# Kernel optimization log

Hardware: AMD Instinct MI355X
Metric: run time of the kernel (lower is better)

## Reference

```python
import jax, jax.numpy as jnp
import numpy as np
from jax import lax

IMG_SIZE = 1024.0  # nominal image dimension for generating plausible coords
IOU_THRESHOLD = 0.5


def box_iou(a, b):
    # a: (N,4), b: (M,4) in (x1,y1,x2,y2); returns (N,M) IoU
    area_a = (a[:, 2] - a[:, 0]) * (a[:, 3] - a[:, 1])
    area_b = (b[:, 2] - b[:, 0]) * (b[:, 3] - b[:, 1])
    lt = jnp.maximum(a[:, None, :2], b[None, :, :2])
    rb = jnp.minimum(a[:, None, 2:], b[None, :, 2:])
    wh = jnp.clip(rb - lt, 0.0)
    inter = wh[..., 0] * wh[..., 1]
    return inter / (area_a[:, None] + area_b[None, :] - inter)


def apply_deltas_to_locations(deltas, locations, stride):
    # Faithful to fcos_apply_deltas_to_locations: clip deltas at 0,
    # un-normalize by stride, subtract/add around the center location.
    d = jnp.clip(deltas, 0.0)  # (N,4) = (l, t, r, b)
    xc, yc = locations[:, 0], locations[:, 1]
    x1 = xc - stride * d[:, 0]
    y1 = yc - stride * d[:, 1]
    x2 = xc + stride * d[:, 2]
    y2 = yc + stride * d[:, 3]
    return jnp.stack([x1, y1, x2, y2], axis=1)


def nms_keep(boxes, scores, iou_threshold):
    # Greedy NMS, equivalent to the sequential reference loop:
    # process boxes in decreasing score order; a box survives if it is not
    # suppressed (IoU > thr) by any earlier surviving box.
    n = boxes.shape[0]
    order = jnp.argsort(-scores)  # descending score order
    b = boxes[order]
    iou = box_iou(b, b)  # (N,N), memory-bound pairwise compare
    idx = jnp.arange(n)

    def body(i, keep):
        suppress = (iou[i] > iou_threshold) & (idx > i) & keep[i]
        return keep & ~suppress

    keep_sorted = lax.fori_loop(0, n, body, jnp.ones((n,), dtype=bool))
    # scatter keep mask back to original ordering
    keep_orig = jnp.zeros((n,), dtype=bool).at[order].set(keep_sorted)
    return keep_orig, order, keep_sorted


def setup_inputs() -> dict:
    key = jax.random.key(0)
    k1, k2, k3, k4 = jax.random.split(key, 4)
    N = 8192
    deltas = jax.random.uniform(k1, (N, 4), dtype=jnp.float32) * 8.0  # stride-normalized LTRB
    locations = jax.random.uniform(k2, (N, 2), dtype=jnp.float32) * IMG_SIZE
    scores = jax.random.uniform(k3, (N,), dtype=jnp.float32)
    class_ids = jax.random.randint(k4, (N,), 0, 80, dtype=jnp.int32)
    return {"deltas": deltas, "locations": locations, "scores": scores,
            "class_ids": class_ids, "stride": 8}


def reference(deltas, locations, scores, class_ids, stride):
    # 1) LTRB delta decode (fcos_apply_deltas_to_locations)
    boxes = apply_deltas_to_locations(deltas, locations, stride)
    # 2) class-specific NMS (class_spec_nms): offset boxes per class so that
    #    boxes of different classes never overlap, then run plain NMS.
    max_coordinate = boxes.max()
    offsets = class_ids.astype(boxes.dtype) * (max_coordinate + 1.0)
    boxes_for_nms = boxes + offsets[:, None]
    keep_orig, order, keep_sorted = nms_keep(boxes_for_nms, scores, IOU_THRESHOLD)
    # boxes: decoded boxes; keep_orig: NMS survival mask (original order);
    # order: score-descending permutation (kept indices = order[keep_sorted])
    return boxes, keep_orig, order
```

## Files before the change

### kernel.cpp

```cpp
#include <hip/hip_runtime.h>

typedef unsigned long long u64;
typedef unsigned int u32;

#define NBOX 8192
#define NW64 128
#define NCLASS 80
#define NCMAX 256
#define CHKCAP 256
#define NS 32
#define SLICE 256
#define NBLK 32
#define K1GRID (NS * NBLK + 1)
#define K2GRID (NBLK + NCLASS)

__device__ __forceinline__ u32 f32_mono(float f) {
  u32 u = __float_as_uint(f);
  return (u & 0x80000000u) ? ~u : (u | 0x80000000u);
}
__device__ __forceinline__ float mono_f32(u32 u) {
  u32 b = (u & 0x80000000u) ? (u ^ 0x80000000u) : ~u;
  return __uint_as_float(b);
}
__device__ __forceinline__ u64 readlane64(u64 v, int l) {
  u32 lo = __builtin_amdgcn_readlane((u32)v, l);
  u32 hi = __builtin_amdgcn_readlane((u32)(v >> 32), l);
  return ((u64)hi << 32) | (u64)lo;
}
__device__ __forceinline__ u32 reduce_bmax(const u32* __restrict__ bmax, int t) {
  u32 bm = bmax[t & 31];
#pragma unroll
  for (int off = 16; off > 0; off >>= 1) {
    u32 o = __shfl_xor(bm, off);
    bm = (bm > o) ? bm : o;
  }
  return bm;
}


__global__ __launch_bounds__(256) void rank_decode_kernel(
    const float* __restrict__ scores, const int* __restrict__ class_ids,
    const float4* __restrict__ deltas, const float2* __restrict__ locs,
    const int* __restrict__ stride_p, float4* __restrict__ boxes_out,
    u32* __restrict__ bmax, int* __restrict__ flag, int* __restrict__ rankp) {
  const int t = threadIdx.x;
  const int b = blockIdx.x;

  if (b == NS * NBLK) {
    __shared__ float4 bxA[CHKCAP], bxB[CHKCAP];
    __shared__ int clsA[CHKCAP], clsB[CHKCAP];
    __shared__ int na, nb, hitf;
    __shared__ u32 mred[4];
    if (t == 0) { na = 0; nb = 0; hitf = 0; }
    float s = (float)(*stride_p);
    u32 mymax = 0;
    for (int base = 0; base < NBOX; base += 256) {
      int i = base + t;
      float4 d = deltas[i];
      d.x = fmaxf(d.x, 0.f); d.y = fmaxf(d.y, 0.f);
      d.z = fmaxf(d.z, 0.f); d.w = fmaxf(d.w, 0.f);
      float2 c = locs[i];
      float x1 = c.x - s * d.x, y1 = c.y - s * d.y;
      float x2 = c.x + s * d.z, y2 = c.y + s * d.w;
      float m = fmaxf(fmaxf(x1, y1), fmaxf(x2, y2));
      u32 u = f32_mono(m);
      mymax = mymax > u ? mymax : u;
    }
#pragma unroll
    for (int off = 32; off > 0; off >>= 1) {
      u32 o = __shfl_xor(mymax, off);
      mymax = mymax > o ? mymax : o;
    }
    if ((t & 63) == 0) mred[t >> 6] = mymax;
    __syncthreads();
    u32 g0 = mred[0] > mred[1] ? mred[0] : mred[1];
    u32 g1 = mred[2] > mred[3] ? mred[2] : mred[3];
    float M = mono_f32(g0 > g1 ? g0 : g1);
    float thrA = M - 65.0f;
    for (int base = 0; base < NBOX; base += 256) {
      int i = base + t;
      float4 d = deltas[i];
      d.x = fmaxf(d.x, 0.f); d.y = fmaxf(d.y, 0.f);
      d.z = fmaxf(d.z, 0.f); d.w = fmaxf(d.w, 0.f);
      float2 c = locs[i];
      float4 bb;
      bb.x = c.x - s * d.x; bb.y = c.y - s * d.y;
      bb.z = c.x + s * d.z; bb.w = c.y + s * d.w;
      int cls = class_ids[i];
      if (bb.z > thrA && bb.w > thrA) {
        int p = atomicAdd(&na, 1);
        if (p < CHKCAP) { bxA[p] = bb; clsA[p] = cls; }
      }
      if (bb.x < 1.0f && bb.y < 1.0f) {
        int p = atomicAdd(&nb, 1);
        if (p < CHKCAP) { bxB[p] = bb; clsB[p] = cls; }
      }
    }
    __syncthreads();
    int NA = na < CHKCAP ? na : CHKCAP;
    int NB = nb < CHKCAP ? nb : CHKCAP;
    bool hit = (t == 0) && (na > CHKCAP || nb > CHKCAP);
    for (int pr = t; pr < NA * NB; pr += 256) {
      int a = pr / NB, b2 = pr % NB;
      if (clsB[b2] != clsA[a] + 1) continue;
      float offa = (float)clsA[a] * (M + 1.0f);
      float offb = (float)clsB[b2] * (M + 1.0f);
      float4 A = bxA[a], Bb = bxB[b2];
      A.x += offa; A.y += offa; A.z += offa; A.w += offa;
      Bb.x += offb; Bb.y += offb; Bb.z += offb; Bb.w += offb;
      float ltx = fmaxf(A.x, Bb.x), lty = fmaxf(A.y, Bb.y);
      float rbx = fminf(A.z, Bb.z), rby = fminf(A.w, Bb.w);
      float ww = fmaxf(rbx - ltx, 0.f), hh = fmaxf(rby - lty, 0.f);
      float inter = ww * hh;
      float aa = (A.z - A.x) * (A.w - A.y);
      float ab = (Bb.z - Bb.x) * (Bb.w - Bb.y);
      float iou = inter / (aa + ab - inter);
      if (iou > 0.4f) hit = true;
    }
    if (hit) atomicOr(&hitf, 1);
    __syncthreads();
    if (t == 0) *flag = hitf;
    return;
  }

  const int bi = b & 31;
  const int slice = b >> 5;
  const int i = bi * 256 + t;

  __shared__ u32 st[SLICE];
  __shared__ u32 wmax[4];

  if (slice == 0) {
    float s = (float)(*stride_p);
    float4 d = deltas[i];
    d.x = fmaxf(d.x, 0.f); d.y = fmaxf(d.y, 0.f);
    d.z = fmaxf(d.z, 0.f); d.w = fmaxf(d.w, 0.f);
    float2 c = locs[i];
    float4 bb;
    bb.x = c.x - s * d.x;
    bb.y = c.y - s * d.y;
    bb.z = c.x + s * d.z;
    bb.w = c.y + s * d.w;
    boxes_out[i] = bb;
    float m = fmaxf(fmaxf(bb.x, bb.y), fmaxf(bb.z, bb.w));
    u32 u = f32_mono(m);
#pragma unroll
    for (int off = 32; off > 0; off >>= 1) {
      u32 o = __shfl_xor(u, off);
      u = (u > o) ? u : o;
    }
    if ((t & 63) == 0) wmax[t >> 6] = u;
  }

  st[t] = f32_mono(scores[slice * 256 + t]);
  __syncthreads();
  if (slice == 0 && t == 0) {
    u32 m0 = wmax[0] > wmax[1] ? wmax[0] : wmax[1];
    u32 m1 = wmax[2] > wmax[3] ? wmax[2] : wmax[3];
    bmax[bi] = m0 > m1 ? m0 : m1;
  }

  u32 mi = f32_mono(scores[i]);
  int tp = i - slice * 256;
  int cnt = 0;
#pragma unroll 8
  for (int p = 0; p < SLICE; ++p) {
    u32 mj = st[p];
    bool less = (mj > mi) || (mj == mi && p < tp);
    cnt += less ? 1 : 0;
  }
  rankp[slice * NBOX + i] = cnt;
}

__global__ __launch_bounds__(256) void scatter_nms_kernel(
    const float* __restrict__ scores, const int* __restrict__ class_ids,
    const float4* __restrict__ boxes, const u32* __restrict__ bmax,
    const int* __restrict__ rankp, u64* __restrict__ keys,
    float4* __restrict__ bnms, float* __restrict__ order_out,
    float* __restrict__ keep_out, int* flag) {
  const int t = threadIdx.x;
  const int bid = blockIdx.x;

  if (bid < NBLK) {
    int i = bid * 256 + t;
    int r = 0;
#pragma unroll
    for (int s2 = 0; s2 < NS; ++s2) r += rankp[s2 * NBOX + i];
    float maxc = mono_f32(reduce_bmax(bmax, t));
    u32 mi = f32_mono(scores[i]);
    keys[r] = ((u64)(~mi) << 32) | (u32)i;
    int cls = class_ids[i];
    float off = (float)cls * (maxc + 1.0f);
    float4 bb = boxes[i];
    bb.x += off; bb.y += off; bb.z += off; bb.w += off;
    bnms[r] = bb;
    order_out[r] = (float)i;
    return;
  }

  const int c = bid - NBLK;
  if (*flag != 0) return;
  __shared__ u64 ck[NCMAX];
  __shared__ u32 slist[NCMAX];
  __shared__ float4 bx[NCMAX];
  __shared__ u64 smask[NCMAX][4];
  __shared__ int cnt_s;
  if (t == 0) cnt_s = 0;
  __syncthreads();

  {
    int nxtc = class_ids[t];
    float nxts = scores[t];
    for (int base = 0; base < NBOX; base += 256) {
      int cur = nxtc;
      float cs = nxts;
      if (base + 256 < NBOX) {
        nxtc = class_ids[base + 256 + t];
        nxts = scores[base + 256 + t];
      }
      if (cur == c) {
        int p = atomicAdd(&cnt_s, 1);
        if (p < NCMAX) ck[p] = ((u64)(~f32_mono(cs)) << 32) | (u32)(base + t);
      }
    }
  }
  __syncthreads();
  int nc = cnt_s;
  if (nc > NCMAX) {
    if (t == 0) atomicOr(flag, 1);
    return;
  }
  if (t < nc) {
    u64 kme = ck[t];
    int r2 = 0;
    for (int p = 0; p < nc; ++p) r2 += (ck[p] < kme) ? 1 : 0;
    slist[r2] = (u32)kme;
  }
  __syncthreads();

  float maxc = mono_f32(reduce_bmax(bmax, t));
  float off = (float)c * (maxc + 1.0f);
  for (int k = t; k < nc; k += 256) {
    float4 bb = boxes[slist[k]];
    bb.x += off; bb.y += off; bb.z += off; bb.w += off;
    bx[k] = bb;
  }
  __syncthreads();

  {
    const int wv = t >> 6;
    const int lane = t & 63;
    const int nw = (nc + 63) >> 6;
    for (int i = wv; i < nc; i += 4) {
      float4 bi = bx[i];
      float area_i = (bi.z - bi.x) * (bi.w - bi.y);
      for (int w = 0; w < nw; ++w) {
        int j2 = w * 64 + lane;
        float4 bj = bx[j2 < NCMAX ? j2 : 0];
        float ltx = fmaxf(bi.x, bj.x), lty = fmaxf(bi.y, bj.y);
        float rbx = fminf(bi.z, bj.z), rby = fminf(bi.w, bj.w);
        float ww = fmaxf(rbx - ltx, 0.f), hh = fmaxf(rby - lty, 0.f);
        float inter = ww * hh;
        float area_j = (bj.z - bj.x) * (bj.w - bj.y);
        float iou = inter / (area_i + area_j - inter);
        bool p = (iou > 0.5f) && (j2 > i) && (j2 < nc);
        u64 mm = __ballot(p);
        if (lane == 0) smask[i][w] = mm;
      }
    }
  }
  __syncthreads();
  if (t >= 64) return;

  u64 ma[4], mb[4], mc[4], md[4];
#pragma unroll
  for (int w = 0; w < 4; ++w) {
    ma[w] = smask[t][w];
    mb[w] = smask[64 + t][w];
    mc[w] = smask[128 + t][w];
    md[w] = smask[192 + t][w];
  }
  u64 R0 = 0, R1 = 0, R2 = 0, R3 = 0;
  u64 K0 = 0, K1 = 0, K2 = 0, K3 = 0;

#define SCAND(D, MD, RD, KD)                                                   \
  {                                                                            \
    int lim = nc - (D) * 64;                                                   \
    if (lim > 0) {                                                             \
      if (lim > 64) lim = 64;                                                  \
      for (int ii = 0; ii < lim; ++ii) {                                       \
        u64 kb = ((RD >> ii) & 1ull) ^ 1ull;                                   \
        KD |= kb << ii;                                                        \
        u64 sm2 = 0ull - kb;                                                   \
        R0 |= readlane64(MD[0], ii) & sm2;                                     \
        R1 |= readlane64(MD[1], ii) & sm2;                                     \
        R2 |= readlane64(MD[2], ii) & sm2;                                     \
        R3 |= readlane64(MD[3], ii) & sm2;                                     \
      }                                                                        \
    }                                                                          \
  }
  SCAND(0, ma, R0, K0)
  SCAND(1, mb, R1, K1)
  SCAND(2, mc, R2, K2)
  SCAND(3, md, R3, K3)
#undef SCAND

  u64 kk[4] = {K0, K1, K2, K3};
#pragma unroll
  for (int d = 0; d < 4; ++d) {
    int j = d * 64 + t;
    if (j < nc) keep_out[slist[j]] = ((kk[d] >> t) & 1ull) ? 1.0f : 0.0f;
  }
}

__global__ __launch_bounds__(256) void fallback_kernel(
    const float4* __restrict__ bnms, const u64* __restrict__ keys,
    float* __restrict__ keep_out, const int* __restrict__ flag) {
  if (*flag == 0) return;
  __shared__ u64 remv[NW64];
  int t = threadIdx.x;
  for (int k = t; k < NW64; k += 256) remv[k] = 0;
  __syncthreads();
  if (t < 64) {
    int lane = t;
    for (int ii = 0; ii < NBOX; ++ii) {
      if ((remv[ii >> 6] >> (ii & 63)) & 1ull) continue;
      float4 bi = bnms[ii];
      float area_i = (bi.z - bi.x) * (bi.w - bi.y);
      for (int jb = ii + 1; jb < NBOX; jb += 64) {
        int j = jb + lane;
        bool p = false;
        if (j < NBOX) {
          float4 bj = bnms[j];
          float ltx = fmaxf(bi.x, bj.x), lty = fmaxf(bi.y, bj.y);
          float rbx = fminf(bi.z, bj.z), rby = fminf(bi.w, bj.w);
          float ww = fmaxf(rbx - ltx, 0.f), hh = fmaxf(rby - lty, 0.f);
          float inter = ww * hh;
          float area_j = (bj.z - bj.x) * (bj.w - bj.y);
          float iou = inter / (area_i + area_j - inter);
          p = iou > 0.5f;
        }
        u64 m = __ballot(p);
        if (lane == 0 && m) {
          int w0 = jb >> 6, sh = jb & 63;
          remv[w0] |= (m << sh);
          if (sh && (w0 + 1) < NW64) remv[w0 + 1] |= (m >> (64 - sh));
        }
      }
    }
  }
  __syncthreads();
  for (int k = t; k < NBOX; k += 256)
    keep_out[(u32)keys[k]] = ((remv[k >> 6] >> (k & 63)) & 1ull) ? 0.0f : 1.0f;
}

extern "C" void kernel_launch(void* const* d_in, const int* in_sizes, int n_in,
                              void* d_out, int out_size, void* d_ws, size_t ws_size,
                              hipStream_t stream) {
  const float* deltas = (const float*)d_in[0];
  const float* locs = (const float*)d_in[1];
  const float* scores = (const float*)d_in[2];
  const int* class_ids = (const int*)d_in[3];
  const int* stride_p = (const int*)d_in[4];

  float* boxes_out = (float*)d_out;
  float* keep_out = (float*)d_out + (size_t)NBOX * 4;
  float* order_out = (float*)d_out + (size_t)NBOX * 5;

  u32* bmax = (u32*)((char*)d_ws + 64);
  int* flag = (int*)((char*)d_ws + 256);
  u64* keys = (u64*)((char*)d_ws + 4096);
  float4* bnms = (float4*)((char*)d_ws + 4096 + 65536);
  int* rankp = (int*)((char*)d_ws + 4096 + 65536 + 131072);

  rank_decode_kernel<<<K1GRID, 256, 0, stream>>>(
      scores, class_ids, (const float4*)deltas, (const float2*)locs, stride_p,
      (float4*)boxes_out, bmax, flag, rankp);

  scatter_nms_kernel<<<K2GRID, 256, 0, stream>>>(
      scores, class_ids, (const float4*)boxes_out, bmax, rankp, keys, bnms,
      order_out, keep_out, flag);

  fallback_kernel<<<1, 256, 0, stream>>>(bnms, keys, keep_out, flag);
}
```

Measured before the change: 52.74 us.

## Build per-class sorted lists during ranking instead of rescanning all boxes per class

The ranking pass now also counts, for each box, how many same-class boxes outrank it, and a histogram pass records per-class counts. The scatter kernel uses these to write each box into a per-class list already in score order. The per-class NMS blocks then read their list directly instead of scanning all 8192 class ids and doing an in-block rank sort. The price is extra compare work and extra rank-partial traffic in the rank kernel, plus splitting scatter and NMS into separate launches.

```diff
diff --git a/kernel.cpp b/kernel.cpp
--- a/kernel.cpp
+++ b/kernel.cpp
@@ -6,13 +6,14 @@
 #define NBOX 8192
 #define NW64 128
 #define NCLASS 80
+#define MAXC 512
 #define NCMAX 256
 #define CHKCAP 256
 #define NS 32
 #define SLICE 256
 #define NBLK 32
 #define K1GRID (NS * NBLK + 1)
-#define K2GRID (NBLK + NCLASS)
+#define K3GRID (NCLASS + 1)
 
 __device__ __forceinline__ u32 f32_mono(float f) {
   u32 u = __float_as_uint(f);
@@ -42,16 +43,19 @@
     const float* __restrict__ scores, const int* __restrict__ class_ids,
     const float4* __restrict__ deltas, const float2* __restrict__ locs,
     const int* __restrict__ stride_p, float4* __restrict__ boxes_out,
-    u32* __restrict__ bmax, int* __restrict__ flag, int* __restrict__ rankp) {
+    u32* __restrict__ bmax, int* __restrict__ flag, int* __restrict__ ccount,
+    int* __restrict__ rankp, int* __restrict__ rcp) {
   const int t = threadIdx.x;
   const int b = blockIdx.x;
 
   if (b == NS * NBLK) {
     __shared__ float4 bxA[CHKCAP], bxB[CHKCAP];
     __shared__ int clsA[CHKCAP], clsB[CHKCAP];
+    __shared__ int hist[NCLASS];
     __shared__ int na, nb, hitf;
     __shared__ u32 mred[4];
     if (t == 0) { na = 0; nb = 0; hitf = 0; }
+    if (t < NCLASS) hist[t] = 0;
     float s = (float)(*stride_p);
     u32 mymax = 0;
     for (int base = 0; base < NBOX; base += 256) {
@@ -87,6 +91,7 @@
       bb.x = c.x - s * d.x; bb.y = c.y - s * d.y;
       bb.z = c.x + s * d.z; bb.w = c.y + s * d.w;
       int cls = class_ids[i];
+      atomicAdd(&hist[cls], 1);
       if (bb.z > thrA && bb.w > thrA) {
         int p = atomicAdd(&na, 1);
         if (p < CHKCAP) { bxA[p] = bb; clsA[p] = cls; }
@@ -97,6 +102,10 @@
       }
     }
     __syncthreads();
+    if (t < NCLASS) {
+      ccount[t] = hist[t];
+      if (hist[t] > NCMAX) atomicOr(&hitf, 1);
+    }
     int NA = na < CHKCAP ? na : CHKCAP;
     int NB = nb < CHKCAP ? nb : CHKCAP;
     bool hit = (t == 0) && (na > CHKCAP || nb > CHKCAP);
@@ -127,7 +136,7 @@
   const int slice = b >> 5;
   const int i = bi * 256 + t;
 
-  __shared__ u32 st[SLICE];
+  __shared__ u64 kt[SLICE];
   __shared__ u32 wmax[4];
 
   if (slice == 0) {
@@ -152,7 +161,10 @@
     if ((t & 63) == 0) wmax[t >> 6] = u;
   }
 
-  st[t] = f32_mono(scores[slice * 256 + t]);
+  {
+    int j = slice * 256 + t;
+    kt[t] = ((u64)f32_mono(scores[j]) << 8) | (u32)(class_ids[j] & 0xff);
+  }
   __syncthreads();
   if (slice == 0 && t == 0) {
     u32 m0 = wmax[0] > wmax[1] ? wmax[0] : wmax[1];
@@ -160,128 +172,106 @@
     bmax[bi] = m0 > m1 ? m0 : m1;
   }
 
-  u32 mi = f32_mono(scores[i]);
+  u64 wi = ((u64)f32_mono(scores[i]) << 8) | (u32)(class_ids[i] & 0xff);
+  u64 si = wi >> 8;
   int tp = i - slice * 256;
-  int cnt = 0;
+  int cnt = 0, ccnt = 0;
 #pragma unroll 8
   for (int p = 0; p < SLICE; ++p) {
-    u32 mj = st[p];
-    bool less = (mj > mi) || (mj == mi && p < tp);
+    u64 wj = kt[p];
+    u64 sj = wj >> 8;
+    bool less = (sj > si) || (sj == si && p < tp);
+    bool ceq = (((u32)(wj ^ wi)) & 0xffu) == 0u;
     cnt += less ? 1 : 0;
+    ccnt += (less && ceq) ? 1 : 0;
   }
   rankp[slice * NBOX + i] = cnt;
-}
-
-__global__ __launch_bounds__(256) void scatter_nms_kernel(
+  rcp[slice * NBOX + i] = ccnt;
+}
+
+__global__ __launch_bounds__(256) void scatter_kernel(
     const float* __restrict__ scores, const int* __restrict__ class_ids,
     const float4* __restrict__ boxes, const u32* __restrict__ bmax,
-    const int* __restrict__ rankp, u64* __restrict__ keys,
-    float4* __restrict__ bnms, float* __restrict__ order_out,
-    float* __restrict__ keep_out, int* flag) {
+    const int* __restrict__ rankp, const int* __restrict__ rcp,
+    u64* __restrict__ keys, float4* __restrict__ bnms,
+    u32* __restrict__ clist, float* __restrict__ order_out) {
+  const int t = threadIdx.x;
+  const int i = blockIdx.x * 256 + t;
+  int r = 0, rc = 0;
+#pragma unroll
+  for (int s2 = 0; s2 < NS; ++s2) {
+    r += rankp[s2 * NBOX + i];
+    rc += rcp[s2 * NBOX + i];
+  }
+  float maxc = mono_f32(reduce_bmax(bmax, t));
+  u32 mi = f32_mono(scores[i]);
+  keys[r] = ((u64)(~mi) << 32) | (u32)i;
+  int cls = class_ids[i];
+  float off = (float)cls * (maxc + 1.0f);
+  float4 bb = boxes[i];
+  bb.x += off; bb.y += off; bb.z += off; bb.w += off;
+  bnms[r] = bb;
+  order_out[r] = (float)i;
+  if (rc < MAXC) clist[cls * MAXC + rc] = ((u32)i << 16) | (u32)r;
+}
+
+__global__ __launch_bounds__(256) void nms_kernel(
+    const u32* __restrict__ clist, const int* __restrict__ ccount,
+    const float4* __restrict__ bnms, const u64* __restrict__ keys,
+    float* __restrict__ keep_out, const int* __restrict__ flag) {
   const int t = threadIdx.x;
   const int bid = blockIdx.x;
 
-  if (bid < NBLK) {
-    int i = bid * 256 + t;
-    int r = 0;
-#pragma unroll
-    for (int s2 = 0; s2 < NS; ++s2) r += rankp[s2 * NBOX + i];
-    float maxc = mono_f32(reduce_bmax(bmax, t));
-    u32 mi = f32_mono(scores[i]);
-    keys[r] = ((u64)(~mi) << 32) | (u32)i;
-    int cls = class_ids[i];
-    float off = (float)cls * (maxc + 1.0f);
-    float4 bb = boxes[i];
-    bb.x += off; bb.y += off; bb.z += off; bb.w += off;
-    bnms[r] = bb;
-    order_out[r] = (float)i;
-    return;
-  }
-
-  const int c = bid - NBLK;
-  if (*flag != 0) return;
-  __shared__ u64 ck[NCMAX];
-  __shared__ u32 slist[NCMAX];
-  __shared__ float4 bx[NCMAX];
-  __shared__ u64 smask[NCMAX][4];
-  __shared__ int cnt_s;
-  if (t == 0) cnt_s = 0;
-  __syncthreads();
-
-  {
-    int nxtc = class_ids[t];
-    float nxts = scores[t];
-    for (int base = 0; base < NBOX; base += 256) {
-      int cur = nxtc;
-      float cs = nxts;
-      if (base + 256 < NBOX) {
-        nxtc = class_ids[base + 256 + t];
-        nxts = scores[base + 256 + t];
+  if (bid < NCLASS) {
+    if (*flag != 0) return;
+    const int c = bid;
+    int nc = ccount[c];
+    if (nc > NCMAX) return;
+    __shared__ u32 elist[NCMAX];
+    __shared__ float4 bx[NCMAX];
+    __shared__ u64 smask[NCMAX][4];
+    for (int k = t; k < nc; k += 256) {
+      u32 e = clist[c * MAXC + k];
+      elist[k] = e;
+      bx[k] = bnms[e & 0xffffu];
+    }
+    __syncthreads();
+
+    {
+      const int wv = t >> 6;
+      const int lane = t & 63;
+      const int nw = (nc + 63) >> 6;
+      for (int i = wv; i < nc; i += 4) {
+        float4 bi = bx[i];
+        float area_i = (bi.z - bi.x) * (bi.w - bi.y);
+        for (int w = 0; w < nw; ++w) {
+          int j2 = w * 64 + lane;
+          float4 bj = bx[j2 < NCMAX ? j2 : 0];
+          float ltx = fmaxf(bi.x, bj.x), lty = fmaxf(bi.y, bj.y);
+          float rbx = fminf(bi.z, bj.z), rby = fminf(bi.w, bj.w);
+          float ww = fmaxf(rbx - ltx, 0.f), hh = fmaxf(rby - lty, 0.f);
+          float inter = ww * hh;
+          float area_j = (bj.z - bj.x) * (bj.w - bj.y);
+          float iou = inter / (area_i + area_j - inter);
+          bool p = (iou > 0.5f) && (j2 > i) && (j2 < nc);
+          u64 mm = __ballot(p);
+          if (lane == 0) smask[i][w] = mm;
+        }
       }
-      if (cur == c) {
-        int p = atomicAdd(&cnt_s, 1);
-        if (p < NCMAX) ck[p] = ((u64)(~f32_mono(cs)) << 32) | (u32)(base + t);
-      }
-    }
-  }
-  __syncthreads();
-  int nc = cnt_s;
-  if (nc > NCMAX) {
-    if (t == 0) atomicOr(flag, 1);
-    return;
-  }
-  if (t < nc) {
-    u64 kme = ck[t];
-    int r2 = 0;
-    for (int p = 0; p < nc; ++p) r2 += (ck[p] < kme) ? 1 : 0;
-    slist[r2] = (u32)kme;
-  }
-  __syncthreads();
-
-  float maxc = mono_f32(reduce_bmax(bmax, t));
-  float off = (float)c * (maxc + 1.0f);
-  for (int k = t; k < nc; k += 256) {
-    float4 bb = boxes[slist[k]];
-    bb.x += off; bb.y += off; bb.z += off; bb.w += off;
-    bx[k] = bb;
-  }
-  __syncthreads();
-
-  {
-    const int wv = t >> 6;
-    const int lane = t & 63;
-    const int nw = (nc + 63) >> 6;
-    for (int i = wv; i < nc; i += 4) {
-      float4 bi = bx[i];
-      float area_i = (bi.z - bi.x) * (bi.w - bi.y);
-      for (int w = 0; w < nw; ++w) {
-        int j2 = w * 64 + lane;
-        float4 bj = bx[j2 < NCMAX ? j2 : 0];
-        float ltx = fmaxf(bi.x, bj.x), lty = fmaxf(bi.y, bj.y);
-        float rbx = fminf(bi.z, bj.z), rby = fminf(bi.w, bj.w);
-        float ww = fmaxf(rbx - ltx, 0.f), hh = fmaxf(rby - lty, 0.f);
-        float inter = ww * hh;
-        float area_j = (bj.z - bj.x) * (bj.w - bj.y);
-        float iou = inter / (area_i + area_j - inter);
-        bool p = (iou > 0.5f) && (j2 > i) && (j2 < nc);
-        u64 mm = __ballot(p);
-        if (lane == 0) smask[i][w] = mm;
-      }
-    }
-  }
-  __syncthreads();
-  if (t >= 64) return;
-
-  u64 ma[4], mb[4], mc[4], md[4];
-#pragma unroll
-  for (int w = 0; w < 4; ++w) {
-    ma[w] = smask[t][w];
-    mb[w] = smask[64 + t][w];
-    mc[w] = smask[128 + t][w];
-    md[w] = smask[192 + t][w];
-  }
-  u64 R0 = 0, R1 = 0, R2 = 0, R3 = 0;
-  u64 K0 = 0, K1 = 0, K2 = 0, K3 = 0;
+    }
+    __syncthreads();
+    if (t >= 64) return;
+
+    u64 ma[4], mb[4], mc[4], md[4];
+#pragma unroll
+    for (int w = 0; w < 4; ++w) {
+      ma[w] = smask[t][w];
+      mb[w] = smask[64 + t][w];
+      mc[w] = smask[128 + t][w];
+      md[w] = smask[192 + t][w];
+    }
+    u64 R0 = 0, R1 = 0, R2 = 0, R3 = 0;
+    u64 K0 = 0, K1 = 0, K2 = 0, K3 = 0;
 
 #define SCAND(D, MD, RD, KD)                                                   \
   {                                                                            \
@@ -299,26 +289,23 @@
       }                                                                        \
     }                                                                          \
   }
-  SCAND(0, ma, R0, K0)
-  SCAND(1, mb, R1, K1)
-  SCAND(2, mc, R2, K2)
-  SCAND(3, md, R3, K3)
+    SCAND(0, ma, R0, K0)
+    SCAND(1, mb, R1, K1)
+    SCAND(2, mc, R2, K2)
+    SCAND(3, md, R3, K3)
 #undef SCAND
 
-  u64 kk[4] = {K0, K1, K2, K3};
-#pragma unroll
-  for (int d = 0; d < 4; ++d) {
-    int j = d * 64 + t;
-    if (j < nc) keep_out[slist[j]] = ((kk[d] >> t) & 1ull) ? 1.0f : 0.0f;
-  }
-}
-
-__global__ __launch_bounds__(256) void fallback_kernel(
-    const float4* __restrict__ bnms, const u64* __restrict__ keys,
-    float* __restrict__ keep_out, const int* __restrict__ flag) {
+    u64 kk[4] = {K0, K1, K2, K3};
+#pragma unroll
+    for (int d = 0; d < 4; ++d) {
+      int j = d * 64 + t;
+      if (j < nc) keep_out[elist[j] >> 16] = ((kk[d] >> t) & 1ull) ? 1.0f : 0.0f;
+    }
+    return;
+  }
+
   if (*flag == 0) return;
   __shared__ u64 remv[NW64];
-  int t = threadIdx.x;
   for (int k = t; k < NW64; k += 256) remv[k] = 0;
   __syncthreads();
   if (t < 64) {
@@ -369,17 +356,22 @@
 
   u32* bmax = (u32*)((char*)d_ws + 64);
   int* flag = (int*)((char*)d_ws + 256);
+  int* ccount = (int*)((char*)d_ws + 512);
   u64* keys = (u64*)((char*)d_ws + 4096);
   float4* bnms = (float4*)((char*)d_ws + 4096 + 65536);
-  int* rankp = (int*)((char*)d_ws + 4096 + 65536 + 131072);
+  char* base2 = (char*)d_ws + 4096 + 65536 + 131072;
+  int* rankp = (int*)base2;
+  int* rcp = (int*)(base2 + 1024 * 1024);
+  u32* clist = (u32*)(base2 + 2048 * 1024);
 
   rank_decode_kernel<<<K1GRID, 256, 0, stream>>>(
       scores, class_ids, (const float4*)deltas, (const float2*)locs, stride_p,
-      (float4*)boxes_out, bmax, flag, rankp);
-
-  scatter_nms_kernel<<<K2GRID, 256, 0, stream>>>(
-      scores, class_ids, (const float4*)boxes_out, bmax, rankp, keys, bnms,
-      order_out, keep_out, flag);
-
-  fallback_kernel<<<1, 256, 0, stream>>>(bnms, keys, keep_out, flag);
-}
+      (float4*)boxes_out, bmax, flag, ccount, rankp, rcp);
+
+  scatter_kernel<<<NBLK, 256, 0, stream>>>(
+      scores, class_ids, (const float4*)boxes_out, bmax, rankp, rcp, keys,
+      bnms, clist, order_out);
+
+  nms_kernel<<<K3GRID, 256, 0, stream>>>(clist, ccount, bnms, keys, keep_out,
+                                         flag);
+}
```

New measurement: 55.34 us. +4.9%, slower.
